# Optimization experiments

Measured on AMD Instinct MI355X. Metric: run time of the kernel, lower is better.

Reference implementation:

```python
import jax, jax.numpy as jnp
import numpy as np

N = 50000   # nodes
E = 800000  # edges (avg degree 16)
H = 128     # hidden


def setup_inputs() -> dict:
    key = jax.random.key(0)
    k1, k2, k3, k4, k5 = jax.random.split(key, 5)
    s = 1.0 / np.sqrt(H).astype(np.float32)
    x = jax.random.normal(k1, (N, H), dtype=jnp.float32)
    edge_index = jax.random.randint(k2, (2, E), 0, N, dtype=jnp.int64)
    a_i = jax.random.normal(k3, (H,), dtype=jnp.float32) * s
    a_j = jax.random.normal(k4, (H,), dtype=jnp.float32) * s
    W = jax.random.normal(k5, (H, H), dtype=jnp.float32) * s
    return {"x": x, "edge_index": edge_index, "a_i": a_i, "a_j": a_j, "W": W}


def reference(x, edge_index, a_i, a_j, W):
    n = x.shape[0]
    idx_j = edge_index[0]  # row of sparse adj (output node)
    idx_i = edge_index[1]  # col of sparse adj (source node, softmax segment)

    # per-node attention scores, gathered per edge
    si = x @ a_i  # [N]
    sj = x @ a_j  # [N]
    e = jax.nn.leaky_relu(si[idx_i] + sj[idx_j], negative_slope=0.01)  # [E]

    # segment softmax over idx_i (numerically stable)
    seg_max = jax.ops.segment_max(e, idx_i, num_segments=n)
    e_exp = jnp.exp(e - seg_max[idx_i])
    denom = jax.ops.segment_sum(e_exp, idx_i, num_segments=n)
    alpha = e_exp / denom[idx_i]  # [E]

    # messages and sparse aggregation: out[j] += alpha * m[i]
    m = x + x @ W  # [N, H]
    out = jax.ops.segment_sum(alpha[:, None] * m[idx_i], idx_j, num_segments=n)

    # exact (erf) GELU to match torch nn.GELU default; dropout is identity in eval
    return jax.nn.gelu(out, approximate=False)
```

## Files before the change

### kernel.cpp

```cpp
#include <hip/hip_runtime.h>
#include <hip/hip_fp16.h>
#include <math.h>

#define HDIM 128
#define NB   32
#define CAP  768
#define BINB 256
#define DG   64
#define WIN  12544

typedef __attribute__((ext_vector_type(8))) short short8;
typedef __attribute__((ext_vector_type(4))) float f32x4;

__device__ __forceinline__ float gelu_f(float v) {
    return 0.5f * v * (1.0f + erff(v * 0.70710678118654752440f));
}
__device__ __forceinline__ unsigned bf_rne(float f) {
    unsigned u = __float_as_uint(f);
    return (u + 0x7fffu + ((u >> 16) & 1u)) >> 16;
}
__device__ __forceinline__ float bf_lo(unsigned u) {
    return __uint_as_float(u << 16);
}
__device__ __forceinline__ float bf_hi(unsigned u) {
    return __uint_as_float(u & 0xffff0000u);
}

__global__ void __launch_bounds__(256) k_scores(
    const float* __restrict__ x, const float* __restrict__ a_i,
    const float* __restrict__ a_j, float* __restrict__ si,
    float* __restrict__ sj, unsigned* __restrict__ xbp, int N) {
    const int wave = threadIdx.x >> 6;
    const int lane = threadIdx.x & 63;
    const int n = blockIdx.x * 4 + wave;
    if (n >= N) return;
    const float xa = x[(size_t)n * HDIM + lane];
    const float xb = x[(size_t)n * HDIM + 64 + lane];
    xbp[(size_t)n * 64 + lane] = bf_rne(xa) | (bf_rne(xb) << 16);
    float vi = xa * a_i[lane] + xb * a_i[64 + lane];
    float vj = xa * a_j[lane] + xb * a_j[64 + lane];
    #pragma unroll
    for (int d = 32; d; d >>= 1) {
        vi += __shfl_xor(vi, d, 64);
        vj += __shfl_xor(vj, d, 64);
    }
    if (lane == 0) {
        si[n] = vi;
        sj[n] = vj;
    }
}

__global__ void __launch_bounds__(1024) k_binA(
    const int* __restrict__ idx_i, const int* __restrict__ idx_j,
    const float* __restrict__ si, const float* __restrict__ sj,
    unsigned short* __restrict__ exbuf, unsigned* __restrict__ cnt_g,
    int nbuk, int E_) {
    __shared__ unsigned cnt_l[2048];
    const int blk = blockIdx.x;
    const int chunk = (E_ + BINB - 1) / BINB;
    const int e0 = blk * chunk;
    const int e1 = min(e0 + chunk, E_);
    for (int w = threadIdx.x; w < nbuk; w += 1024) cnt_l[w] = 0u;
    __syncthreads();
    for (int t = e0 + threadIdx.x; t < e1; t += 1024) {
        const int i = idx_i[t];
        const int j = idx_j[t];
        float e = si[i] + sj[j];
        e = (e > 0.f) ? e : 0.01f * e;
        const float ex = __expf(e);
        exbuf[t] = __half_as_ushort(__float2half(ex));
        atomicAdd(&cnt_l[j >> 5], 1u);
    }
    __syncthreads();
    for (int w = threadIdx.x; w < nbuk; w += 1024)
        cnt_g[(size_t)blk * nbuk + w] = cnt_l[w];
}

__global__ void __launch_bounds__(256) k_scan(
    const unsigned* __restrict__ cnt_g, unsigned* __restrict__ base_t,
    unsigned* __restrict__ gcnt, int nbuk) {
    const int bucket = blockIdx.x;
    const int t = threadIdx.x;
    const int lane = t & 63;
    const int wave = t >> 6;
    const unsigned v = cnt_g[(size_t)t * nbuk + bucket];
    unsigned s = v;
    #pragma unroll
    for (int d = 1; d < 64; d <<= 1) {
        const unsigned o = __shfl_up(s, d, 64);
        if (lane >= d) s += o;
    }
    __shared__ unsigned wsum[4];
    if (lane == 63) wsum[wave] = s;
    __syncthreads();
    unsigned add = 0;
    #pragma unroll
    for (int w = 0; w < 4; ++w)
        if (w < wave) add += wsum[w];
    base_t[(size_t)t * nbuk + bucket] = add + s - v;
    if (t == 255) gcnt[bucket] = add + s;
}

__global__ void __launch_bounds__(1024) k_den(
    const int* __restrict__ idx_i, const unsigned short* __restrict__ exbuf,
    float* __restrict__ denp, int N, int E_) {
    __shared__ float dl[WIN];
    const int cid = blockIdx.x & (DG - 1);
    const int lo = (blockIdx.x >> 6) * WIN;
    const int chunk = (E_ + DG - 1) / DG;
    const int e0 = cid * chunk;
    const int e1 = min(e0 + chunk, E_);
    for (int w = threadIdx.x; w < WIN; w += 1024) dl[w] = 0.f;
    __syncthreads();
    for (int t = e0 + threadIdx.x; t < e1; t += 1024) {
        const unsigned rel = (unsigned)(idx_i[t] - lo);
        if (rel < (unsigned)WIN)
            atomicAdd(&dl[rel], __half2float(__ushort_as_half(exbuf[t])));
    }
    __syncthreads();
    for (int w = threadIdx.x; w < WIN && lo + w < N; w += 1024)
        denp[(size_t)cid * N + lo + w] = dl[w];
}

__global__ void __launch_bounds__(256) k_denred(const float* __restrict__ denp,
                                                float* __restrict__ denom,
                                                int N) {
    const int v = blockIdx.x * 256 + threadIdx.x;
    if (v >= N) return;
    float s = 0.f;
    for (int b = 0; b < DG; ++b) s += denp[(size_t)b * N + v];
    denom[v] = s;
}

__global__ void __launch_bounds__(1024) k_binB(
    const int* __restrict__ idx_i, const int* __restrict__ idx_j,
    const unsigned short* __restrict__ exbuf,
    const float* __restrict__ denom, const unsigned* __restrict__ base_t,
    uint2* __restrict__ edges, int nbuk, int E_) {
    __shared__ unsigned cur[2048];
    const int blk = blockIdx.x;
    const int chunk = (E_ + BINB - 1) / BINB;
    const int e0 = blk * chunk;
    const int e1 = min(e0 + chunk, E_);
    for (int w = threadIdx.x; w < nbuk; w += 1024)
        cur[w] = base_t[(size_t)blk * nbuk + w];
    __syncthreads();
    for (int t = e0 + threadIdx.x; t < e1; t += 1024) {
        const int i = idx_i[t];
        const int j = idx_j[t];
        const float ex = __half2float(__ushort_as_half(exbuf[t]));
        const float alpha = ex / denom[i];
        const int b = j >> 5;
        const unsigned slot = min(atomicAdd(&cur[b], 1u), (unsigned)(CAP - 1));
        edges[(size_t)b * CAP + slot] = make_uint2(
            (unsigned)i | ((unsigned)(j & 31) << 24), __float_as_uint(alpha));
    }
}

__global__ void __launch_bounds__(512) k_agg(
    const unsigned* __restrict__ gcnt, const uint2* __restrict__ edges,
    const unsigned* __restrict__ xbp, unsigned* __restrict__ sbp, int N) {
    __shared__ uint2 srec[CAP];
    __shared__ unsigned cnt_l[NB];
    __shared__ unsigned off_l[NB];
    const int b = blockIdx.x;
    const int cntb = min((int)gcnt[b], CAP);
    const uint2* eb = edges + (size_t)b * CAP;
    if (threadIdx.x < NB) cnt_l[threadIdx.x] = 0u;
    __syncthreads();
    uint2 r0_ = make_uint2(0u, 0u), r1_ = make_uint2(0u, 0u);
    int jl0 = -1, jl1 = -1, kl0 = 0, kl1 = 0;
    {
        const int t0 = threadIdx.x;
        if (t0 < cntb) {
            r0_ = eb[t0];
            jl0 = (int)(r0_.x >> 24);
            kl0 = (int)atomicAdd(&cnt_l[jl0], 1u);
        }
        const int t1 = threadIdx.x + 512;
        if (t1 < cntb) {
            r1_ = eb[t1];
            jl1 = (int)(r1_.x >> 24);
            kl1 = (int)atomicAdd(&cnt_l[jl1], 1u);
        }
    }
    __syncthreads();
    if (threadIdx.x < NB) {
        const unsigned v = cnt_l[threadIdx.x];
        unsigned s = v;
        #pragma unroll
        for (int d = 1; d < NB; d <<= 1) {
            const unsigned o = __shfl_up(s, d, 64);
            if ((int)threadIdx.x >= d) s += o;
        }
        off_l[threadIdx.x] = s - v;
    }
    __syncthreads();
    if (jl0 >= 0) srec[off_l[jl0] + kl0] = r0_;
    if (jl1 >= 0) srec[off_l[jl1] + kl1] = r1_;
    __syncthreads();
    const int wave = threadIdx.x >> 6;
    const int lane = threadIdx.x & 63;
    for (int nr = wave; nr < NB; nr += 8) {
        const int n = (b << 5) + nr;
        if (n >= N) continue;
        const int p0 = (int)off_l[nr];
        const int p1 = p0 + (int)cnt_l[nr];
        float ax = 0.f, ay = 0.f;
        int p = p0;
        for (; p + 8 <= p1; p += 8) {
            const uint2 e0 = srec[p];
            const uint2 e1 = srec[p + 1];
            const uint2 e2 = srec[p + 2];
            const uint2 e3 = srec[p + 3];
            const uint2 e4 = srec[p + 4];
            const uint2 e5 = srec[p + 5];
            const uint2 e6 = srec[p + 6];
            const uint2 e7 = srec[p + 7];
            const unsigned u0 = xbp[(size_t)(e0.x & 0xffffffu) * 64 + lane];
            const unsigned u1 = xbp[(size_t)(e1.x & 0xffffffu) * 64 + lane];
            const unsigned u2 = xbp[(size_t)(e2.x & 0xffffffu) * 64 + lane];
            const unsigned u3 = xbp[(size_t)(e3.x & 0xffffffu) * 64 + lane];
            const unsigned u4 = xbp[(size_t)(e4.x & 0xffffffu) * 64 + lane];
            const unsigned u5 = xbp[(size_t)(e5.x & 0xffffffu) * 64 + lane];
            const unsigned u6 = xbp[(size_t)(e6.x & 0xffffffu) * 64 + lane];
            const unsigned u7 = xbp[(size_t)(e7.x & 0xffffffu) * 64 + lane];
            ax = fmaf(__uint_as_float(e0.y), bf_lo(u0), ax);
            ay = fmaf(__uint_as_float(e0.y), bf_hi(u0), ay);
            ax = fmaf(__uint_as_float(e1.y), bf_lo(u1), ax);
            ay = fmaf(__uint_as_float(e1.y), bf_hi(u1), ay);
            ax = fmaf(__uint_as_float(e2.y), bf_lo(u2), ax);
            ay = fmaf(__uint_as_float(e2.y), bf_hi(u2), ay);
            ax = fmaf(__uint_as_float(e3.y), bf_lo(u3), ax);
            ay = fmaf(__uint_as_float(e3.y), bf_hi(u3), ay);
            ax = fmaf(__uint_as_float(e4.y), bf_lo(u4), ax);
            ay = fmaf(__uint_as_float(e4.y), bf_hi(u4), ay);
            ax = fmaf(__uint_as_float(e5.y), bf_lo(u5), ax);
            ay = fmaf(__uint_as_float(e5.y), bf_hi(u5), ay);
            ax = fmaf(__uint_as_float(e6.y), bf_lo(u6), ax);
            ay = fmaf(__uint_as_float(e6.y), bf_hi(u6), ay);
            ax = fmaf(__uint_as_float(e7.y), bf_lo(u7), ax);
            ay = fmaf(__uint_as_float(e7.y), bf_hi(u7), ay);
        }
        for (; p + 4 <= p1; p += 4) {
            const uint2 e0 = srec[p];
            const uint2 e1 = srec[p + 1];
            const uint2 e2 = srec[p + 2];
            const uint2 e3 = srec[p + 3];
            const unsigned u0 = xbp[(size_t)(e0.x & 0xffffffu) * 64 + lane];
            const unsigned u1 = xbp[(size_t)(e1.x & 0xffffffu) * 64 + lane];
            const unsigned u2 = xbp[(size_t)(e2.x & 0xffffffu) * 64 + lane];
            const unsigned u3 = xbp[(size_t)(e3.x & 0xffffffu) * 64 + lane];
            ax = fmaf(__uint_as_float(e0.y), bf_lo(u0), ax);
            ay = fmaf(__uint_as_float(e0.y), bf_hi(u0), ay);
            ax = fmaf(__uint_as_float(e1.y), bf_lo(u1), ax);
            ay = fmaf(__uint_as_float(e1.y), bf_hi(u1), ay);
            ax = fmaf(__uint_as_float(e2.y), bf_lo(u2), ax);
            ay = fmaf(__uint_as_float(e2.y), bf_hi(u2), ay);
            ax = fmaf(__uint_as_float(e3.y), bf_lo(u3), ax);
            ay = fmaf(__uint_as_float(e3.y), bf_hi(u3), ay);
        }
        for (; p < p1; ++p) {
            const uint2 e = srec[p];
            const unsigned u = xbp[(size_t)(e.x & 0xffffffu) * 64 + lane];
            const float a = __uint_as_float(e.y);
            ax = fmaf(a, bf_lo(u), ax);
            ay = fmaf(a, bf_hi(u), ay);
        }
        sbp[(size_t)n * 64 + lane] = bf_rne(ax) | (bf_rne(ay) << 16);
    }
}

__global__ void __launch_bounds__(256) k_out(
    const unsigned* __restrict__ sbp, const float* __restrict__ Wm,
    float* __restrict__ out, int N) {
    __shared__ unsigned wl[128][68];
    const int t = threadIdx.x;
    {
        const int n = t & 127;
        const int h = t >> 7;
        for (int w = h * 32; w < h * 32 + 32; ++w) {
            const float f0 = Wm[w * 128 + n];
            const float f1 = Wm[(w + 64) * 128 + n];
            wl[n][w] = bf_rne(f0) | (bf_rne(f1) << 16);
        }
    }
    __syncthreads();
    const int wave = t >> 6;
    const int lane = t & 63;
    const int q = lane >> 4;
    const int m16 = lane & 15;
    const int r0 = blockIdx.x * 64 + wave * 16;
    if (r0 >= N) return;
    const int rowA = min(r0 + m16, N - 1);
    union { uint4 u; short8 s; } a[4];
    #pragma unroll
    for (int kb = 0; kb < 4; ++kb)
        a[kb].u = *(const uint4*)(sbp + (size_t)rowA * 64 + kb * 16 + q * 4);
    f32x4 acc[8];
    #pragma unroll
    for (int c = 0; c < 8; ++c) acc[c] = (f32x4){0.f, 0.f, 0.f, 0.f};
    #pragma unroll
    for (int kb = 0; kb < 4; ++kb) {
        #pragma unroll
        for (int c = 0; c < 8; ++c) {
            const short8 bfr =
                *(const short8*)&wl[c * 16 + m16][kb * 16 + q * 4];
            acc[c] = __builtin_amdgcn_mfma_f32_16x16x32_bf16(
                a[kb].s, bfr, acc[c], 0, 0, 0);
        }
    }
    #pragma unroll
    for (int r = 0; r < 4; ++r) {
        const int row = r0 + q * 4 + r;
        if (row >= N) continue;
        #pragma unroll
        for (int c = 0; c < 4; ++c) {
            const int w = m16 + 16 * c;
            const unsigned sv = sbp[(size_t)row * 64 + w];
            const float vlo = bf_lo(sv) + acc[c][r];
            const float vhi = bf_hi(sv) + acc[c + 4][r];
            out[(size_t)row * HDIM + w] = gelu_f(vlo);
            out[(size_t)row * HDIM + w + 64] = gelu_f(vhi);
        }
    }
}

extern "C" void kernel_launch(void* const* d_in, const int* in_sizes, int n_in,
                              void* d_out, int out_size, void* d_ws,
                              size_t ws_size, hipStream_t stream) {
    const float* x   = (const float*)d_in[0];
    const int*   eix = (const int*)d_in[1];
    const float* a_i = (const float*)d_in[2];
    const float* a_j = (const float*)d_in[3];
    const float* Wm  = (const float*)d_in[4];
    float* out = (float*)d_out;

    const int N = in_sizes[0] / HDIM;
    const int E = in_sizes[1] / 2;
    const int nbuk = (N + NB - 1) / NB;

    unsigned* xbp   = (unsigned*)d_ws;
    unsigned* sbp   = xbp + (size_t)N * 64;
    float* denp     = (float*)(sbp + (size_t)N * 64);
    float* si       = denp + (size_t)DG * N;
    float* sj       = si + N;
    float* denom    = sj + N;
    unsigned* cnt_g = (unsigned*)(denom + N);
    unsigned* base_t = cnt_g + (size_t)BINB * nbuk;
    unsigned* gcnt  = base_t + (size_t)BINB * nbuk;
    unsigned short* exbuf =
        (unsigned short*)(gcnt + ((nbuk + 7) & ~7));
    uint2* edges    = (uint2*)(exbuf + ((E + 7) & ~7));

    const int* idx_j = eix;
    const int* idx_i = eix + E;

    k_scores<<<(N + 3) / 4, 256, 0, stream>>>(x, a_i, a_j, si, sj, xbp, N);
    k_binA<<<BINB, 1024, 0, stream>>>(idx_i, idx_j, si, sj, exbuf, cnt_g,
                                      nbuk, E);
    k_scan<<<nbuk, 256, 0, stream>>>(cnt_g, base_t, gcnt, nbuk);
    k_den<<<DG * 4, 1024, 0, stream>>>(idx_i, exbuf, denp, N, E);
    k_denred<<<(N + 255) / 256, 256, 0, stream>>>(denp, denom, N);
    k_binB<<<BINB, 1024, 0, stream>>>(idx_i, idx_j, exbuf, denom, base_t,
                                      edges, nbuk, E);
    k_agg<<<nbuk, 512, 0, stream>>>(gcnt, edges, xbp, sbp, N);
    k_out<<<(N + 63) / 64, 256, 0, stream>>>(sbp, Wm, out, N);
}
```

Measured before the change: 174.0 us.

## Fuse aggregation with W-matmul and GELU output into one kernel

Merges the aggregation kernel and the MFMA output kernel into a single 1024-thread kernel. Aggregated rows stay in shared memory instead of making a bf16 round trip through a global buffer. Bucket size grows from 32 to 64 nodes (capacity 1536) so each block covers a 64-row MFMA tile. The cost is more shared memory per block and a W conversion redone in every block, which may lower occupancy. Fewer blocks also risks bucket overflow being clamped at the cap.

```diff
diff --git a/kernel.cpp b/kernel.cpp
--- a/kernel.cpp
+++ b/kernel.cpp
@@ -3,8 +3,8 @@
 #include <math.h>
 
 #define HDIM 128
-#define NB   32
-#define CAP  768
+#define NB   64
+#define CAP  1536
 #define BINB 256
 #define DG   64
 #define WIN  12544
@@ -55,7 +55,7 @@
     const float* __restrict__ si, const float* __restrict__ sj,
     unsigned short* __restrict__ exbuf, unsigned* __restrict__ cnt_g,
     int nbuk, int E_) {
-    __shared__ unsigned cnt_l[2048];
+    __shared__ unsigned cnt_l[1024];
     const int blk = blockIdx.x;
     const int chunk = (E_ + BINB - 1) / BINB;
     const int e0 = blk * chunk;
@@ -69,7 +69,7 @@
         e = (e > 0.f) ? e : 0.01f * e;
         const float ex = __expf(e);
         exbuf[t] = __half_as_ushort(__float2half(ex));
-        atomicAdd(&cnt_l[j >> 5], 1u);
+        atomicAdd(&cnt_l[j >> 6], 1u);
     }
     __syncthreads();
     for (int w = threadIdx.x; w < nbuk; w += 1024)
@@ -137,7 +137,7 @@
     const unsigned short* __restrict__ exbuf,
     const float* __restrict__ denom, const unsigned* __restrict__ base_t,
     uint2* __restrict__ edges, int nbuk, int E_) {
-    __shared__ unsigned cur[2048];
+    __shared__ unsigned cur[1024];
     const int blk = blockIdx.x;
     const int chunk = (E_ + BINB - 1) / BINB;
     const int e0 = blk * chunk;
@@ -150,60 +150,67 @@
         const int j = idx_j[t];
         const float ex = __half2float(__ushort_as_half(exbuf[t]));
         const float alpha = ex / denom[i];
-        const int b = j >> 5;
+        const int b = j >> 6;
         const unsigned slot = min(atomicAdd(&cur[b], 1u), (unsigned)(CAP - 1));
         edges[(size_t)b * CAP + slot] = make_uint2(
-            (unsigned)i | ((unsigned)(j & 31) << 24), __float_as_uint(alpha));
-    }
-}
-
-__global__ void __launch_bounds__(512) k_agg(
+            (unsigned)i | ((unsigned)(j & 63) << 24), __float_as_uint(alpha));
+    }
+}
+
+__global__ void __launch_bounds__(1024) k_aggout(
     const unsigned* __restrict__ gcnt, const uint2* __restrict__ edges,
-    const unsigned* __restrict__ xbp, unsigned* __restrict__ sbp, int N) {
+    const unsigned* __restrict__ xbp, const float* __restrict__ Wm,
+    float* __restrict__ out, int N) {
+    __shared__ __align__(16) unsigned wl[128][68];
+    __shared__ __align__(16) unsigned s_l[64][68];
     __shared__ uint2 srec[CAP];
     __shared__ unsigned cnt_l[NB];
     __shared__ unsigned off_l[NB];
     const int b = blockIdx.x;
+    const int t = threadIdx.x;
     const int cntb = min((int)gcnt[b], CAP);
     const uint2* eb = edges + (size_t)b * CAP;
-    if (threadIdx.x < NB) cnt_l[threadIdx.x] = 0u;
+    if (t < NB) cnt_l[t] = 0u;
     __syncthreads();
     uint2 r0_ = make_uint2(0u, 0u), r1_ = make_uint2(0u, 0u);
     int jl0 = -1, jl1 = -1, kl0 = 0, kl1 = 0;
+    if (t < cntb) {
+        r0_ = eb[t];
+        jl0 = (int)(r0_.x >> 24);
+        kl0 = (int)atomicAdd(&cnt_l[jl0], 1u);
+    }
+    if (t + 1024 < cntb) {
+        r1_ = eb[t + 1024];
+        jl1 = (int)(r1_.x >> 24);
+        kl1 = (int)atomicAdd(&cnt_l[jl1], 1u);
+    }
     {
-        const int t0 = threadIdx.x;
-        if (t0 < cntb) {
-            r0_ = eb[t0];
-            jl0 = (int)(r0_.x >> 24);
-            kl0 = (int)atomicAdd(&cnt_l[jl0], 1u);
-        }
-        const int t1 = threadIdx.x + 512;
-        if (t1 < cntb) {
-            r1_ = eb[t1];
-            jl1 = (int)(r1_.x >> 24);
-            kl1 = (int)atomicAdd(&cnt_l[jl1], 1u);
-        }
-    }
-    __syncthreads();
-    if (threadIdx.x < NB) {
-        const unsigned v = cnt_l[threadIdx.x];
+        const int n = t & 127;
+        const int h = t >> 7;
+        #pragma unroll
+        for (int w = h * 8; w < h * 8 + 8; ++w) {
+            wl[n][w] = bf_rne(Wm[w * 128 + n]) |
+                       (bf_rne(Wm[(w + 64) * 128 + n]) << 16);
+        }
+    }
+    __syncthreads();
+    if (t < NB) {
+        const unsigned v = cnt_l[t];
         unsigned s = v;
         #pragma unroll
         for (int d = 1; d < NB; d <<= 1) {
             const unsigned o = __shfl_up(s, d, 64);
-            if ((int)threadIdx.x >= d) s += o;
-        }
-        off_l[threadIdx.x] = s - v;
+            if (t >= d) s += o;
+        }
+        off_l[t] = s - v;
     }
     __syncthreads();
     if (jl0 >= 0) srec[off_l[jl0] + kl0] = r0_;
     if (jl1 >= 0) srec[off_l[jl1] + kl1] = r1_;
     __syncthreads();
-    const int wave = threadIdx.x >> 6;
-    const int lane = threadIdx.x & 63;
-    for (int nr = wave; nr < NB; nr += 8) {
-        const int n = (b << 5) + nr;
-        if (n >= N) continue;
+    const int wave = t >> 6;
+    const int lane = t & 63;
+    for (int nr = wave; nr < NB; nr += 16) {
         const int p0 = (int)off_l[nr];
         const int p1 = p0 + (int)cnt_l[nr];
         float ax = 0.f, ay = 0.f;
@@ -267,61 +274,50 @@
             ax = fmaf(a, bf_lo(u), ax);
             ay = fmaf(a, bf_hi(u), ay);
         }
-        sbp[(size_t)n * 64 + lane] = bf_rne(ax) | (bf_rne(ay) << 16);
-    }
-}
-
-__global__ void __launch_bounds__(256) k_out(
-    const unsigned* __restrict__ sbp, const float* __restrict__ Wm,
-    float* __restrict__ out, int N) {
-    __shared__ unsigned wl[128][68];
-    const int t = threadIdx.x;
-    {
-        const int n = t & 127;
-        const int h = t >> 7;
-        for (int w = h * 32; w < h * 32 + 32; ++w) {
-            const float f0 = Wm[w * 128 + n];
-            const float f1 = Wm[(w + 64) * 128 + n];
-            wl[n][w] = bf_rne(f0) | (bf_rne(f1) << 16);
-        }
-    }
-    __syncthreads();
-    const int wave = t >> 6;
-    const int lane = t & 63;
+        s_l[nr][lane] = bf_rne(ax) | (bf_rne(ay) << 16);
+    }
+    __syncthreads();
+    const int g = wave & 3;
+    const int hh = wave >> 2;
     const int q = lane >> 4;
     const int m16 = lane & 15;
-    const int r0 = blockIdx.x * 64 + wave * 16;
-    if (r0 >= N) return;
-    const int rowA = min(r0 + m16, N - 1);
+    const int r0r = g * 16;
     union { uint4 u; short8 s; } a[4];
     #pragma unroll
     for (int kb = 0; kb < 4; ++kb)
-        a[kb].u = *(const uint4*)(sbp + (size_t)rowA * 64 + kb * 16 + q * 4);
-    f32x4 acc[8];
-    #pragma unroll
-    for (int c = 0; c < 8; ++c) acc[c] = (f32x4){0.f, 0.f, 0.f, 0.f};
+        a[kb].u = *(const uint4*)&s_l[r0r + m16][kb * 16 + q * 4];
+    f32x4 acc[2];
+    #pragma unroll
+    for (int cc = 0; cc < 2; ++cc) acc[cc] = (f32x4){0.f, 0.f, 0.f, 0.f};
     #pragma unroll
     for (int kb = 0; kb < 4; ++kb) {
         #pragma unroll
-        for (int c = 0; c < 8; ++c) {
+        for (int cc = 0; cc < 2; ++cc) {
+            const int cp = hh * 2 + cc;
             const short8 bfr =
-                *(const short8*)&wl[c * 16 + m16][kb * 16 + q * 4];
-            acc[c] = __builtin_amdgcn_mfma_f32_16x16x32_bf16(
-                a[kb].s, bfr, acc[c], 0, 0, 0);
+                *(const short8*)&wl[cp * 16 + m16][kb * 16 + q * 4];
+            acc[cc] = __builtin_amdgcn_mfma_f32_16x16x32_bf16(
+                a[kb].s, bfr, acc[cc], 0, 0, 0);
         }
     }
     #pragma unroll
     for (int r = 0; r < 4; ++r) {
-        const int row = r0 + q * 4 + r;
-        if (row >= N) continue;
+        const int row = r0r + q * 4 + r;
+        const int grow = (b << 6) + row;
+        if (grow >= N) continue;
         #pragma unroll
-        for (int c = 0; c < 4; ++c) {
-            const int w = m16 + 16 * c;
-            const unsigned sv = sbp[(size_t)row * 64 + w];
-            const float vlo = bf_lo(sv) + acc[c][r];
-            const float vhi = bf_hi(sv) + acc[c + 4][r];
-            out[(size_t)row * HDIM + w] = gelu_f(vlo);
-            out[(size_t)row * HDIM + w + 64] = gelu_f(vhi);
+        for (int cc = 0; cc < 2; ++cc) {
+            const int cp = hh * 2 + cc;
+            if (cp < 4) {
+                const int w = m16 + 16 * cp;
+                const unsigned sv = s_l[row][w];
+                out[(size_t)grow * HDIM + w] = gelu_f(bf_lo(sv) + acc[cc][r]);
+            } else {
+                const int w = m16 + 16 * (cp - 4);
+                const unsigned sv = s_l[row][w];
+                out[(size_t)grow * HDIM + w + 64] =
+                    gelu_f(bf_hi(sv) + acc[cc][r]);
+            }
         }
     }
 }
@@ -341,8 +337,7 @@
     const int nbuk = (N + NB - 1) / NB;
 
     unsigned* xbp   = (unsigned*)d_ws;
-    unsigned* sbp   = xbp + (size_t)N * 64;
-    float* denp     = (float*)(sbp + (size_t)N * 64);
+    float* denp     = (float*)(xbp + (size_t)N * 64);
     float* si       = denp + (size_t)DG * N;
     float* sj       = si + N;
     float* denom    = sj + N;
@@ -364,6 +359,5 @@
     k_denred<<<(N + 255) / 256, 256, 0, stream>>>(denp, denom, N);
     k_binB<<<BINB, 1024, 0, stream>>>(idx_i, idx_j, exbuf, denom, base_t,
                                       edges, nbuk, E);
-    k_agg<<<nbuk, 512, 0, stream>>>(gcnt, edges, xbp, sbp, N);
-    k_out<<<(N + 63) / 64, 256, 0, stream>>>(sbp, Wm, out, N);
-}
+    k_aggout<<<nbuk, 1024, 0, stream>>>(gcnt, edges, xbp, Wm, out, N);
+}
```

Measured after the change: 167.1 us. 4.0% less time.
